# Kernel tuning notes

Measured on AMD Instinct MI355X. Metric: run time of the kernel, lower is better.

The kernel has to match this reference:

```python
import jax, jax.numpy as jnp
import numpy as np
import math

B, T, C = 4, 2048, 768
N_HEADS = 12

def setup_inputs() -> dict:
    key = jax.random.key(0)
    k1, k2, k3 = jax.random.split(key, 3)
    s_in = 1.0 / math.sqrt(C)
    x = jax.random.normal(k1, (B, T, C), dtype=jnp.float32)
    w_attn = jax.random.normal(k2, (C, 3 * C), dtype=jnp.float32) * s_in
    b_attn = jnp.zeros((3 * C,), dtype=jnp.float32)
    w_proj = jax.random.normal(k3, (C, C), dtype=jnp.float32) * s_in
    b_proj = jnp.zeros((C,), dtype=jnp.float32)
    return {"x": x, "w_attn": w_attn, "b_attn": b_attn, "w_proj": w_proj, "b_proj": b_proj}

def reference(x, w_attn, b_attn, w_proj, b_proj):
    Bx, Tx, Cx = x.shape
    hd = Cx // N_HEADS  # head_dim
    qkv = x @ w_attn + b_attn                       # [B,T,3C]
    q, k, v = jnp.split(qkv, 3, axis=-1)
    def heads(t):  # [B,T,C] -> [B,H,T,hd]
        return t.reshape(Bx, Tx, N_HEADS, hd).transpose(0, 2, 1, 3)
    q, k, v = heads(q), heads(k), heads(v)
    scores = jnp.einsum('bhqd,bhkd->bhqk', q, k) * (1.0 / math.sqrt(hd))
    causal = jnp.tril(jnp.ones((Tx, Tx), dtype=bool))
    scores = jnp.where(causal, scores, -jnp.inf)
    attn = jax.nn.softmax(scores, axis=-1)
    out = jnp.einsum('bhqk,bhkd->bhqd', attn, v)    # [B,H,T,hd]
    out = out.transpose(0, 2, 1, 3).reshape(Bx, Tx, Cx)
    return out @ w_proj + b_proj
```

## Files before the change

kernel.cpp:

```cpp
#include <hip/hip_runtime.h>
#include <hip/hip_bf16.h>

typedef __bf16 bf16_8 __attribute__((ext_vector_type(8)));
typedef float f32x4 __attribute__((ext_vector_type(4)));
typedef unsigned short us4 __attribute__((ext_vector_type(4)));

#define AS1(p) ((const __attribute__((address_space(1))) void*)(p))
#define AS3(p) ((__attribute__((address_space(3))) void*)(p))

#define Bb 4
#define Tt 2048
#define Cc 768
#define NH 12
#define HD 64
#define Mrows 8192
#define N1 2304
#define KDIM 768
#define QSCALE 0.1803368801111204f

__device__ __forceinline__ unsigned short bfbits(float x) {
    __bf16 h = (__bf16)x;
    return __builtin_bit_cast(unsigned short, h);
}

__device__ __forceinline__ float exp2fast(float x) {
#if __has_builtin(__builtin_amdgcn_exp2f)
    return __builtin_amdgcn_exp2f(x);
#else
    return __expf(0.6931471805599453f * x);
#endif
}

__global__ __launch_bounds__(256) void cast_f32_bf16(const float* __restrict__ in,
                                                     __bf16* __restrict__ out, int n4) {
    int i = blockIdx.x * blockDim.x + threadIdx.x;
    if (i < n4) {
        float4 v = ((const float4*)in)[i];
        us4 o;
        o.x = bfbits(v.x); o.y = bfbits(v.y); o.z = bfbits(v.z); o.w = bfbits(v.w);
        *(us4*)(out + (size_t)i * 4) = o;
    }
}

__global__ __launch_bounds__(256) void transpose_cast(const float* __restrict__ in,
                                                      __bf16* __restrict__ out, int R, int Cn) {
    __shared__ float tile[32][33];
    int c0 = blockIdx.x * 32, r0 = blockIdx.y * 32;
    int tx = threadIdx.x, ty = threadIdx.y;
#pragma unroll
    for (int i = 0; i < 4; ++i)
        tile[ty + i * 8][tx] = in[(size_t)(r0 + ty + i * 8) * Cn + c0 + tx];
    __syncthreads();
#pragma unroll
    for (int i = 0; i < 4; ++i)
        out[(size_t)(c0 + ty + i * 8) * R + r0 + tx] = (__bf16)tile[tx][ty + i * 8];
}

template <int MODE>
__global__ __launch_bounds__(256) void gemm_bt(const __bf16* __restrict__ A,
                                               const __bf16* __restrict__ Bt,
                                               const float* __restrict__ bias,
                                               float* __restrict__ outf,
                                               __bf16* __restrict__ qb,
                                               __bf16* __restrict__ kb,
                                               __bf16* __restrict__ vTb,
                                               int M, int N, int K) {
    __shared__ __bf16 As[2][128 * 32];
    __shared__ __bf16 Bs[2][128 * 32];
    int tid = threadIdx.x;
    int w = tid >> 6, l = tid & 63, lr = l & 15, lg = l >> 4;
    int wm = w >> 1, wn = w & 1;

    int gx = gridDim.x, gy = gridDim.y;
    int nwg = gx * gy;
    int orig = blockIdx.y * gx + blockIdx.x;
    int q8 = nwg >> 3, r8 = nwg & 7;
    int xcd = orig & 7, rest = orig >> 3;
    int swz = (xcd < r8) ? xcd * (q8 + 1) + rest
                         : r8 * (q8 + 1) + (xcd - r8) * q8 + rest;
    int bx = swz / gy, by = swz % gy;
    int m0 = bx * 128, n0 = by * 128;

    f32x4 acc[4][4] = {};

#define GSTAGE(buf, kk) do {                                                                 \
    _Pragma("unroll")                                                                        \
    for (int i_ = 0; i_ < 2; ++i_) {                                                         \
        int c_ = i_ * 256 + tid;                                                             \
        int row_ = c_ >> 2;                                                                  \
        int jc_ = ((c_ & 3) ^ (row_ & 3)) << 3;                                              \
        __builtin_amdgcn_global_load_lds(AS1(A + (size_t)(m0 + row_) * K + (kk) + jc_),      \
                                         AS3(&As[buf][c_ * 8]), 16, 0, 0);                   \
        __builtin_amdgcn_global_load_lds(AS1(Bt + (size_t)(n0 + row_) * K + (kk) + jc_),     \
                                         AS3(&Bs[buf][c_ * 8]), 16, 0, 0);                   \
    }                                                                                        \
} while (0)

    GSTAGE(0, 0);
    asm volatile("s_waitcnt vmcnt(0)" ::: "memory");
    __builtin_amdgcn_sched_barrier(0);
    __builtin_amdgcn_s_barrier();
    __builtin_amdgcn_sched_barrier(0);

    int nkt = K >> 5;
    for (int kt = 0; kt < nkt; ++kt) {
        int cur = kt & 1;
        if (kt + 1 < nkt) {
            GSTAGE(cur ^ 1, (kt + 1) * 32);
            asm volatile("s_waitcnt vmcnt(4)" ::: "memory");
        } else {
            asm volatile("s_waitcnt vmcnt(0)" ::: "memory");
        }
        __builtin_amdgcn_sched_barrier(0);
        __builtin_amdgcn_s_barrier();
        __builtin_amdgcn_sched_barrier(0);

        const __bf16* Ac = &As[cur][0];
        const __bf16* Bc = &Bs[cur][0];
        bf16_8 af[4], bfr[4];
#pragma unroll
        for (int mi = 0; mi < 4; ++mi)
            af[mi] = *(const bf16_8*)&Ac[(wm * 64 + mi * 16 + lr) * 32 +
                                         ((lg ^ (lr & 3)) << 3)];
#pragma unroll
        for (int ni = 0; ni < 4; ++ni)
            bfr[ni] = *(const bf16_8*)&Bc[(wn * 64 + ni * 16 + lr) * 32 +
                                          ((lg ^ (lr & 3)) << 3)];
#pragma unroll
        for (int mi = 0; mi < 4; ++mi)
#pragma unroll
            for (int ni = 0; ni < 4; ++ni)
                acc[mi][ni] = __builtin_amdgcn_mfma_f32_16x16x32_bf16(af[mi], bfr[ni],
                                                                      acc[mi][ni], 0, 0, 0);
        asm volatile("s_waitcnt lgkmcnt(0)" ::: "memory");
        __builtin_amdgcn_sched_barrier(0);
        __builtin_amdgcn_s_barrier();
        __builtin_amdgcn_sched_barrier(0);
    }

#pragma unroll
    for (int ni = 0; ni < 4; ++ni) {
        int gn = n0 + wn * 64 + ni * 16 + lr;
        float bv = bias[gn];
#pragma unroll
        for (int mi = 0; mi < 4; ++mi) {
            int gm0 = m0 + wm * 64 + mi * 16 + lg * 4;
            f32x4 v = acc[mi][ni];
            if (MODE == 1) {
#pragma unroll
                for (int r = 0; r < 4; ++r)
                    outf[(size_t)(gm0 + r) * N + gn] = v[r] + bv;
            } else {
                int seg = gn / Cc;
                int rem = gn - seg * Cc;
                int h = rem >> 6, d = rem & 63;
                int b = gm0 >> 11, t = gm0 & 2047;
                size_t bh = (size_t)b * NH + h;
                if (seg < 2) {
                    float sc = (seg == 0) ? QSCALE : 1.0f;
                    __bf16* dst = (seg ? kb : qb) + (bh * Tt + t) * HD + d;
#pragma unroll
                    for (int r = 0; r < 4; ++r)
                        dst[(size_t)r * HD] = (__bf16)((v[r] + bv) * sc);
                } else {
                    us4 pk;
#pragma unroll
                    for (int r = 0; r < 4; ++r) pk[r] = bfbits(v[r] + bv);
                    *(us4*)(vTb + (bh * HD + d) * Tt + t) = pk;
                }
            }
        }
    }
}

__global__ __launch_bounds__(256, 2) void attn_fwd(const __bf16* __restrict__ q,
                                                   const __bf16* __restrict__ k,
                                                   const __bf16* __restrict__ vT,
                                                   __bf16* __restrict__ aout) {
    __shared__ __bf16 Ks[2][64 * 64];
    __shared__ __bf16 Vs[2][64 * 64];
    __shared__ __bf16 Ps[4][16 * 64];
    const float NEGINF = -__builtin_inff();

    int blk = blockIdx.x;
    int bh = blk % 48;
    int j = blk / 48;
    int qtA = j, qtB = 31 - j;
    int tid = threadIdx.x;
    int w = tid >> 6, l = tid & 63, lr = l & 15, lg = l >> 4;

    const __bf16* qp = q + (size_t)bh * Tt * HD;
    const __bf16* kp = k + (size_t)bh * Tt * HD;
    const __bf16* vp = vT + (size_t)bh * HD * Tt;

    bf16_8 qfA0, qfA1, qfB0, qfB1;
    {
        int q0A = qtA * 64 + w * 16, q0B = qtB * 64 + w * 16;
        qfA0 = *(const bf16_8*)(qp + (size_t)(q0A + lr) * HD + lg * 8);
        qfA1 = *(const bf16_8*)(qp + (size_t)(q0A + lr) * HD + 32 + lg * 8);
        qfB0 = *(const bf16_8*)(qp + (size_t)(q0B + lr) * HD + lg * 8);
        qfB1 = *(const bf16_8*)(qp + (size_t)(q0B + lr) * HD + 32 + lg * 8);
    }

    f32x4 accOA[4] = {}, accOB[4] = {};
    float sA[4] = {}, sB[4] = {};

    const int swz = lr & 7;
    const int co0 = (lg ^ swz) * 8;
    const int co1 = ((4 + lg) ^ swz) * 8;
    const int qloc = w * 16 + lg * 4;
    __bf16* Pw = &Ps[w][0];

#define STAGE(buf, kvbase) do {                                                              \
    int c0_ = tid, c1_ = 256 + tid;                                                          \
    int row0_ = c0_ >> 3, j0_ = (c0_ & 7) ^ (row0_ & 7);                                     \
    int row1_ = c1_ >> 3, j1_ = (c1_ & 7) ^ (row1_ & 7);                                     \
    __builtin_amdgcn_global_load_lds(AS1(kp + (size_t)((kvbase) + row0_) * HD + j0_ * 8),    \
                                     AS3(&Ks[buf][c0_ * 8]), 16, 0, 0);                      \
    __builtin_amdgcn_global_load_lds(AS1(vp + (size_t)row0_ * Tt + (kvbase) + j0_ * 8),      \
                                     AS3(&Vs[buf][c0_ * 8]), 16, 0, 0);                      \
    __builtin_amdgcn_global_load_lds(AS1(kp + (size_t)((kvbase) + row1_) * HD + j1_ * 8),    \
                                     AS3(&Ks[buf][c1_ * 8]), 16, 0, 0);                      \
    __builtin_amdgcn_global_load_lds(AS1(vp + (size_t)row1_ * Tt + (kvbase) + j1_ * 8),      \
                                     AS3(&Vs[buf][c1_ * 8]), 16, 0, 0);                      \
} while (0)

#define TILE_COMPUTE(qf0, qf1, accO, s, diag) do {                                           \
    f32x4 accS_[4] = {};                                                                     \
    __builtin_amdgcn_s_setprio(1);                                                           \
    _Pragma("unroll")                                                                        \
    for (int nt = 0; nt < 4; ++nt) {                                                         \
        int rb = (nt * 16 + lr) * 64;                                                        \
        bf16_8 kf0_ = *(const bf16_8*)(Kc_ + rb + co0);                                      \
        bf16_8 kf1_ = *(const bf16_8*)(Kc_ + rb + co1);                                      \
        accS_[nt] = __builtin_amdgcn_mfma_f32_16x16x32_bf16(qf0, kf0_, accS_[nt], 0, 0, 0);  \
        accS_[nt] = __builtin_amdgcn_mfma_f32_16x16x32_bf16(qf1, kf1_, accS_[nt], 0, 0, 0);  \
    }                                                                                        \
    __builtin_amdgcn_s_setprio(0);                                                           \
    if (diag) {                                                                              \
        _Pragma("unroll")                                                                    \
        for (int nt = 0; nt < 4; ++nt) {                                                     \
            int kloc_ = nt * 16 + lr;                                                        \
            _Pragma("unroll")                                                                \
            for (int r = 0; r < 4; ++r)                                                      \
                if (kloc_ > qloc + r) accS_[nt][r] = NEGINF;                                 \
        }                                                                                    \
    }                                                                                        \
    _Pragma("unroll")                                                                        \
    for (int r = 0; r < 4; ++r) {                                                            \
        int prow_ = lg * 4 + r;                                                              \
        _Pragma("unroll")                                                                    \
        for (int nt = 0; nt < 4; ++nt) {                                                     \
            float pv_ = exp2fast(accS_[nt][r]);                                              \
            s[r] += pv_;                                                                     \
            int col_ = nt * 16 + lr;                                                         \
            Pw[prow_ * 64 + (((col_ >> 3) ^ (prow_ & 7)) << 3) + (col_ & 7)] = (__bf16)pv_;  \
        }                                                                                    \
    }                                                                                        \
    bf16_8 pf0_ = *(const bf16_8*)&Pw[lr * 64 + ((lg ^ swz) << 3)];                          \
    bf16_8 pf1_ = *(const bf16_8*)&Pw[lr * 64 + (((4 + lg) ^ swz) << 3)];                    \
    __builtin_amdgcn_s_setprio(1);                                                           \
    _Pragma("unroll")                                                                        \
    for (int dt = 0; dt < 4; ++dt) {                                                         \
        int rb = (dt * 16 + lr) * 64;                                                        \
        bf16_8 vf0_ = *(const bf16_8*)(Vc_ + rb + co0);                                      \
        bf16_8 vf1_ = *(const bf16_8*)(Vc_ + rb + co1);                                      \
        accO[dt] = __builtin_amdgcn_mfma_f32_16x16x32_bf16(pf0_, vf0_, accO[dt], 0, 0, 0);   \
        accO[dt] = __builtin_amdgcn_mfma_f32_16x16x32_bf16(pf1_, vf1_, accO[dt], 0, 0, 0);   \
    }                                                                                        \
    __builtin_amdgcn_s_setprio(0);                                                           \
} while (0)

    STAGE(0, 0);
    asm volatile("s_waitcnt vmcnt(0)" ::: "memory");
    __builtin_amdgcn_sched_barrier(0);
    __builtin_amdgcn_s_barrier();
    __builtin_amdgcn_sched_barrier(0);

    for (int kv = 0; kv <= qtB; ++kv) {
        int cur = kv & 1;
        if (kv < qtB) {
            STAGE(cur ^ 1, (kv + 1) * 64);
            asm volatile("s_waitcnt vmcnt(4)" ::: "memory");
        } else {
            asm volatile("s_waitcnt vmcnt(0)" ::: "memory");
        }
        __builtin_amdgcn_sched_barrier(0);
        __builtin_amdgcn_s_barrier();
        __builtin_amdgcn_sched_barrier(0);

        const __bf16* Kc_ = &Ks[cur][0];
        const __bf16* Vc_ = &Vs[cur][0];
        TILE_COMPUTE(qfB0, qfB1, accOB, sB, kv == qtB);
        if (kv <= qtA)
            TILE_COMPUTE(qfA0, qfA1, accOA, sA, kv == qtA);

        asm volatile("s_waitcnt lgkmcnt(0)" ::: "memory");
        __builtin_amdgcn_sched_barrier(0);
        __builtin_amdgcn_s_barrier();
        __builtin_amdgcn_sched_barrier(0);
    }

    int b = bh / NH, h = bh - b * NH;
#define EPILOGUE(accO, s, qt) do {                                                           \
    _Pragma("unroll")                                                                        \
    for (int r = 0; r < 4; ++r) {                                                            \
        float ss_ = s[r];                                                                    \
        _Pragma("unroll")                                                                    \
        for (int off = 1; off < 16; off <<= 1)                                               \
            ss_ += __shfl_xor(ss_, off);                                                     \
        float inv_ = 1.0f / ss_;                                                             \
        size_t row_ = (size_t)(b * Tt + (qt) * 64 + w * 16 + lg * 4 + r) * Cc + h * HD;      \
        _Pragma("unroll")                                                                    \
        for (int dt = 0; dt < 4; ++dt)                                                       \
            aout[row_ + dt * 16 + lr] = (__bf16)(accO[dt][r] * inv_);                        \
    }                                                                                        \
} while (0)

    EPILOGUE(accOA, sA, qtA);
    EPILOGUE(accOB, sB, qtB);
}

extern "C" void kernel_launch(void* const* d_in, const int* in_sizes, int n_in,
                              void* d_out, int out_size, void* d_ws, size_t ws_size,
                              hipStream_t stream) {
    const float* x      = (const float*)d_in[0];
    const float* w_attn = (const float*)d_in[1];
    const float* b_attn = (const float*)d_in[2];
    const float* w_proj = (const float*)d_in[3];
    const float* b_proj = (const float*)d_in[4];
    float* out = (float*)d_out;

    char* ws = (char*)d_ws;
    constexpr size_t SZ_XB   = (size_t)Mrows * KDIM * 2;
    constexpr size_t SZ_WAT  = (size_t)N1 * KDIM * 2;
    constexpr size_t SZ_WPT  = (size_t)Cc * Cc * 2;
    constexpr size_t SZ_HEAD = (size_t)Bb * NH * Tt * HD * 2;
    __bf16* xb  = (__bf16*)ws;
    __bf16* wat = (__bf16*)(ws + SZ_XB);
    __bf16* wpt = (__bf16*)(ws + SZ_XB + SZ_WAT);
    __bf16* qb  = (__bf16*)(ws + SZ_XB + SZ_WAT + SZ_WPT);
    __bf16* kb  = (__bf16*)(ws + SZ_XB + SZ_WAT + SZ_WPT + SZ_HEAD);
    __bf16* vTb = (__bf16*)(ws + SZ_XB + SZ_WAT + SZ_WPT + 2 * SZ_HEAD);
    __bf16* ao  = (__bf16*)(ws + SZ_XB + SZ_WAT + SZ_WPT + 3 * SZ_HEAD);

    cast_f32_bf16<<<(Mrows * KDIM / 4 + 255) / 256, 256, 0, stream>>>(x, xb, Mrows * KDIM / 4);
    transpose_cast<<<dim3(N1 / 32, KDIM / 32), dim3(32, 8), 0, stream>>>(w_attn, wat, KDIM, N1);
    transpose_cast<<<dim3(Cc / 32, Cc / 32), dim3(32, 8), 0, stream>>>(w_proj, wpt, Cc, Cc);

    gemm_bt<0><<<dim3(Mrows / 128, N1 / 128), 256, 0, stream>>>(
        xb, wat, b_attn, nullptr, qb, kb, vTb, Mrows, N1, KDIM);

    attn_fwd<<<48 * 16, 256, 0, stream>>>(qb, kb, vTb, ao);

    gemm_bt<1><<<dim3(Mrows / 128, Cc / 128), 256, 0, stream>>>(
        ao, wpt, b_proj, out, nullptr, nullptr, nullptr, Mrows, Cc, KDIM);
}
```

Baseline: 133.4 us.

## Enlarge attention query tiles to 128 rows and stage QKV epilogue through LDS

The attention kernel now gives each wave 32 query rows instead of 16, so every block covers two 128-row query tiles and the grid is halved. Each K/V tile loaded into LDS is therefore reused across twice as many queries. The causal mask now uses global indices and covers the two diagonal KV tiles. Separately, the QKV GEMM epilogue for the Q and K segments writes through LDS so it can emit 16-byte coalesced stores, replacing scattered 2-byte stores. The cost is higher register pressure, fewer blocks for load balancing, and an extra LDS pass in the GEMM epilogue.

```diff
diff --git a/kernel.cpp b/kernel.cpp
--- a/kernel.cpp
+++ b/kernel.cpp
@@ -65,8 +65,7 @@
                                                __bf16* __restrict__ kb,
                                                __bf16* __restrict__ vTb,
                                                int M, int N, int K) {
-    __shared__ __bf16 As[2][128 * 32];
-    __shared__ __bf16 Bs[2][128 * 32];
+    __shared__ __bf16 SMEM[4][128 * 32];
     int tid = threadIdx.x;
     int w = tid >> 6, l = tid & 63, lr = l & 15, lg = l >> 4;
     int wm = w >> 1, wn = w & 1;
@@ -90,9 +89,9 @@
         int row_ = c_ >> 2;                                                                  \
         int jc_ = ((c_ & 3) ^ (row_ & 3)) << 3;                                              \
         __builtin_amdgcn_global_load_lds(AS1(A + (size_t)(m0 + row_) * K + (kk) + jc_),      \
-                                         AS3(&As[buf][c_ * 8]), 16, 0, 0);                   \
+                                         AS3(&SMEM[buf][c_ * 8]), 16, 0, 0);                 \
         __builtin_amdgcn_global_load_lds(AS1(Bt + (size_t)(n0 + row_) * K + (kk) + jc_),     \
-                                         AS3(&Bs[buf][c_ * 8]), 16, 0, 0);                   \
+                                         AS3(&SMEM[2 + (buf)][c_ * 8]), 16, 0, 0);           \
     }                                                                                        \
 } while (0)
 
@@ -115,8 +114,8 @@
         __builtin_amdgcn_s_barrier();
         __builtin_amdgcn_sched_barrier(0);
 
-        const __bf16* Ac = &As[cur][0];
-        const __bf16* Bc = &Bs[cur][0];
+        const __bf16* Ac = &SMEM[cur][0];
+        const __bf16* Bc = &SMEM[2 + cur][0];
         bf16_8 af[4], bfr[4];
 #pragma unroll
         for (int mi = 0; mi < 4; ++mi)
@@ -138,31 +137,55 @@
         __builtin_amdgcn_sched_barrier(0);
     }
 
-#pragma unroll
-    for (int ni = 0; ni < 4; ++ni) {
-        int gn = n0 + wn * 64 + ni * 16 + lr;
-        float bv = bias[gn];
-#pragma unroll
-        for (int mi = 0; mi < 4; ++mi) {
-            int gm0 = m0 + wm * 64 + mi * 16 + lg * 4;
-            f32x4 v = acc[mi][ni];
-            if (MODE == 1) {
+    int seg = (MODE == 0) ? (n0 / Cc) : 0;
+    if (MODE == 0 && seg < 2) {
+        __bf16* Cs = &SMEM[0][0];
+        float sc = (seg == 0) ? QSCALE : 1.0f;
+#pragma unroll
+        for (int ni = 0; ni < 4; ++ni) {
+            int lnn = wn * 64 + ni * 16 + lr;
+            float bv = bias[n0 + lnn];
+#pragma unroll
+            for (int mi = 0; mi < 4; ++mi) {
+                int lm0 = wm * 64 + mi * 16 + lg * 4;
+                f32x4 v = acc[mi][ni];
 #pragma unroll
                 for (int r = 0; r < 4; ++r)
-                    outf[(size_t)(gm0 + r) * N + gn] = v[r] + bv;
-            } else {
-                int seg = gn / Cc;
-                int rem = gn - seg * Cc;
-                int h = rem >> 6, d = rem & 63;
-                int b = gm0 >> 11, t = gm0 & 2047;
-                size_t bh = (size_t)b * NH + h;
-                if (seg < 2) {
-                    float sc = (seg == 0) ? QSCALE : 1.0f;
-                    __bf16* dst = (seg ? kb : qb) + (bh * Tt + t) * HD + d;
+                    Cs[(lm0 + r) * 128 + lnn] = (__bf16)((v[r] + bv) * sc);
+            }
+        }
+        __builtin_amdgcn_s_barrier();
+        __bf16* base = seg ? kb : qb;
+        int nrem = n0 - seg * Cc;
+#pragma unroll
+        for (int i = 0; i < 8; ++i) {
+            int c = i * 256 + tid;
+            int lm = c >> 4, ln8 = (c & 15) << 3;
+            int t = m0 + lm;
+            int b = t >> 11, tt = t & 2047;
+            int col = nrem + ln8;
+            int h = col >> 6, d = col & 63;
+            *(bf16_8*)(base + ((size_t)(b * NH + h) * Tt + tt) * HD + d) =
+                *(const bf16_8*)&Cs[lm * 128 + ln8];
+        }
+    } else {
+#pragma unroll
+        for (int ni = 0; ni < 4; ++ni) {
+            int gn = n0 + wn * 64 + ni * 16 + lr;
+            float bv = bias[gn];
+#pragma unroll
+            for (int mi = 0; mi < 4; ++mi) {
+                int gm0 = m0 + wm * 64 + mi * 16 + lg * 4;
+                f32x4 v = acc[mi][ni];
+                if (MODE == 1) {
 #pragma unroll
                     for (int r = 0; r < 4; ++r)
-                        dst[(size_t)r * HD] = (__bf16)((v[r] + bv) * sc);
+                        outf[(size_t)(gm0 + r) * N + gn] = v[r] + bv;
                 } else {
+                    int rem = gn - 2 * Cc;
+                    int h = rem >> 6, d = rem & 63;
+                    int b = gm0 >> 11, t = gm0 & 2047;
+                    size_t bh = (size_t)b * NH + h;
                     us4 pk;
 #pragma unroll
                     for (int r = 0; r < 4; ++r) pk[r] = bfbits(v[r] + bv);
@@ -179,36 +202,36 @@
                                                    __bf16* __restrict__ aout) {
     __shared__ __bf16 Ks[2][64 * 64];
     __shared__ __bf16 Vs[2][64 * 64];
-    __shared__ __bf16 Ps[4][16 * 64];
+    __shared__ __bf16 Ps[4][32 * 64];
     const float NEGINF = -__builtin_inff();
 
     int blk = blockIdx.x;
     int bh = blk % 48;
     int j = blk / 48;
-    int qtA = j, qtB = 31 - j;
+    int jA = j, jB = 15 - j;
     int tid = threadIdx.x;
     int w = tid >> 6, l = tid & 63, lr = l & 15, lg = l >> 4;
+    int wb = w * 32;
 
     const __bf16* qp = q + (size_t)bh * Tt * HD;
     const __bf16* kp = k + (size_t)bh * Tt * HD;
     const __bf16* vp = vT + (size_t)bh * HD * Tt;
 
-    bf16_8 qfA0, qfA1, qfB0, qfB1;
-    {
-        int q0A = qtA * 64 + w * 16, q0B = qtB * 64 + w * 16;
-        qfA0 = *(const bf16_8*)(qp + (size_t)(q0A + lr) * HD + lg * 8);
-        qfA1 = *(const bf16_8*)(qp + (size_t)(q0A + lr) * HD + 32 + lg * 8);
-        qfB0 = *(const bf16_8*)(qp + (size_t)(q0B + lr) * HD + lg * 8);
-        qfB1 = *(const bf16_8*)(qp + (size_t)(q0B + lr) * HD + 32 + lg * 8);
-    }
-
-    f32x4 accOA[4] = {}, accOB[4] = {};
-    float sA[4] = {}, sB[4] = {};
+    bf16_8 qfA[2][2], qfB[2][2];
+#pragma unroll
+    for (int mf = 0; mf < 2; ++mf)
+#pragma unroll
+        for (int ks = 0; ks < 2; ++ks) {
+            qfA[mf][ks] = *(const bf16_8*)(qp + (size_t)(jA * 128 + wb + mf * 16 + lr) * HD + ks * 32 + lg * 8);
+            qfB[mf][ks] = *(const bf16_8*)(qp + (size_t)(jB * 128 + wb + mf * 16 + lr) * HD + ks * 32 + lg * 8);
+        }
+
+    f32x4 accOA[2][4] = {}, accOB[2][4] = {};
+    float sA[2][4] = {}, sB[2][4] = {};
 
     const int swz = lr & 7;
     const int co0 = (lg ^ swz) * 8;
     const int co1 = ((4 + lg) ^ swz) * 8;
-    const int qloc = w * 16 + lg * 4;
     __bf16* Pw = &Ps[w][0];
 
 #define STAGE(buf, kvbase) do {                                                              \
@@ -225,48 +248,65 @@
                                      AS3(&Vs[buf][c1_ * 8]), 16, 0, 0);                      \
 } while (0)
 
-#define TILE_COMPUTE(qf0, qf1, accO, s, diag) do {                                           \
-    f32x4 accS_[4] = {};                                                                     \
+#define TILE9(qf, accO, s, qbase, kvb, domask) do {                                          \
+    f32x4 accS_[2][4] = {};                                                                  \
     __builtin_amdgcn_s_setprio(1);                                                           \
     _Pragma("unroll")                                                                        \
     for (int nt = 0; nt < 4; ++nt) {                                                         \
         int rb = (nt * 16 + lr) * 64;                                                        \
         bf16_8 kf0_ = *(const bf16_8*)(Kc_ + rb + co0);                                      \
         bf16_8 kf1_ = *(const bf16_8*)(Kc_ + rb + co1);                                      \
-        accS_[nt] = __builtin_amdgcn_mfma_f32_16x16x32_bf16(qf0, kf0_, accS_[nt], 0, 0, 0);  \
-        accS_[nt] = __builtin_amdgcn_mfma_f32_16x16x32_bf16(qf1, kf1_, accS_[nt], 0, 0, 0);  \
+        _Pragma("unroll")                                                                    \
+        for (int mf = 0; mf < 2; ++mf) {                                                     \
+            accS_[mf][nt] = __builtin_amdgcn_mfma_f32_16x16x32_bf16(qf[mf][0], kf0_, accS_[mf][nt], 0, 0, 0); \
+            accS_[mf][nt] = __builtin_amdgcn_mfma_f32_16x16x32_bf16(qf[mf][1], kf1_, accS_[mf][nt], 0, 0, 0); \
+        }                                                                                    \
     }                                                                                        \
     __builtin_amdgcn_s_setprio(0);                                                           \
-    if (diag) {                                                                              \
+    if (domask) {                                                                            \
         _Pragma("unroll")                                                                    \
         for (int nt = 0; nt < 4; ++nt) {                                                     \
-            int kloc_ = nt * 16 + lr;                                                        \
+            int kg_ = (kvb) + nt * 16 + lr;                                                  \
             _Pragma("unroll")                                                                \
-            for (int r = 0; r < 4; ++r)                                                      \
-                if (kloc_ > qloc + r) accS_[nt][r] = NEGINF;                                 \
+            for (int mf = 0; mf < 2; ++mf) {                                                 \
+                int qg_ = (qbase) + mf * 16 + lg * 4;                                        \
+                _Pragma("unroll")                                                            \
+                for (int r = 0; r < 4; ++r)                                                  \
+                    if (kg_ > qg_ + r) accS_[mf][nt][r] = NEGINF;                            \
+            }                                                                                \
         }                                                                                    \
     }                                                                                        \
     _Pragma("unroll")                                                                        \
-    for (int r = 0; r < 4; ++r) {                                                            \
-        int prow_ = lg * 4 + r;                                                              \
+    for (int mf = 0; mf < 2; ++mf) {                                                         \
         _Pragma("unroll")                                                                    \
-        for (int nt = 0; nt < 4; ++nt) {                                                     \
-            float pv_ = exp2fast(accS_[nt][r]);                                              \
-            s[r] += pv_;                                                                     \
-            int col_ = nt * 16 + lr;                                                         \
-            Pw[prow_ * 64 + (((col_ >> 3) ^ (prow_ & 7)) << 3) + (col_ & 7)] = (__bf16)pv_;  \
+        for (int r = 0; r < 4; ++r) {                                                        \
+            int prow_ = mf * 16 + lg * 4 + r;                                                \
+            _Pragma("unroll")                                                                \
+            for (int nt = 0; nt < 4; ++nt) {                                                 \
+                float pv_ = exp2fast(accS_[mf][nt][r]);                                      \
+                s[mf][r] += pv_;                                                             \
+                int col_ = nt * 16 + lr;                                                     \
+                Pw[prow_ * 64 + (((col_ >> 3) ^ (prow_ & 7)) << 3) + (col_ & 7)] = (__bf16)pv_; \
+            }                                                                                \
         }                                                                                    \
     }                                                                                        \
-    bf16_8 pf0_ = *(const bf16_8*)&Pw[lr * 64 + ((lg ^ swz) << 3)];                          \
-    bf16_8 pf1_ = *(const bf16_8*)&Pw[lr * 64 + (((4 + lg) ^ swz) << 3)];                    \
+    bf16_8 pf_[2][2];                                                                        \
+    _Pragma("unroll")                                                                        \
+    for (int mf = 0; mf < 2; ++mf) {                                                         \
+        pf_[mf][0] = *(const bf16_8*)&Pw[(mf * 16 + lr) * 64 + ((lg ^ swz) << 3)];           \
+        pf_[mf][1] = *(const bf16_8*)&Pw[(mf * 16 + lr) * 64 + (((4 + lg) ^ swz) << 3)];     \
+    }                                                                                        \
     __builtin_amdgcn_s_setprio(1);                                                           \
     _Pragma("unroll")                                                                        \
     for (int dt = 0; dt < 4; ++dt) {                                                         \
         int rb = (dt * 16 + lr) * 64;                                                        \
         bf16_8 vf0_ = *(const bf16_8*)(Vc_ + rb + co0);                                      \
         bf16_8 vf1_ = *(const bf16_8*)(Vc_ + rb + co1);                                      \
-        accO[dt] = __builtin_amdgcn_mfma_f32_16x16x32_bf16(pf0_, vf0_, accO[dt], 0, 0, 0);   \
-        accO[dt] = __builtin_amdgcn_mfma_f32_16x16x32_bf16(pf1_, vf1_, accO[dt], 0, 0, 0);   \
+        _Pragma("unroll")                                                                    \
+        for (int mf = 0; mf < 2; ++mf) {                                                     \
+            accO[mf][dt] = __builtin_amdgcn_mfma_f32_16x16x32_bf16(pf_[mf][0], vf0_, accO[mf][dt], 0, 0, 0); \
+            accO[mf][dt] = __builtin_amdgcn_mfma_f32_16x16x32_bf16(pf_[mf][1], vf1_, accO[mf][dt], 0, 0, 0); \
+        }                                                                                    \
     }                                                                                        \
     __builtin_amdgcn_s_setprio(0);                                                           \
 } while (0)
@@ -277,9 +317,10 @@
     __builtin_amdgcn_s_barrier();
     __builtin_amdgcn_sched_barrier(0);
 
-    for (int kv = 0; kv <= qtB; ++kv) {
+    int nkv = 32 - 2 * j;
+    for (int kv = 0; kv < nkv; ++kv) {
         int cur = kv & 1;
-        if (kv < qtB) {
+        if (kv + 1 < nkv) {
             STAGE(cur ^ 1, (kv + 1) * 64);
             asm volatile("s_waitcnt vmcnt(4)" ::: "memory");
         } else {
@@ -291,9 +332,9 @@
 
         const __bf16* Kc_ = &Ks[cur][0];
         const __bf16* Vc_ = &Vs[cur][0];
-        TILE_COMPUTE(qfB0, qfB1, accOB, sB, kv == qtB);
-        if (kv <= qtA)
-            TILE_COMPUTE(qfA0, qfA1, accOA, sA, kv == qtA);
+        TILE9(qfB, accOB, sB, jB * 128 + wb, kv * 64, kv >= 2 * jB);
+        if (kv <= 2 * jA + 1)
+            TILE9(qfA, accOA, sA, jA * 128 + wb, kv * 64, kv >= 2 * jA);
 
         asm volatile("s_waitcnt lgkmcnt(0)" ::: "memory");
         __builtin_amdgcn_sched_barrier(0);
@@ -302,23 +343,26 @@
     }
 
     int b = bh / NH, h = bh - b * NH;
-#define EPILOGUE(accO, s, qt) do {                                                           \
-    _Pragma("unroll")                                                                        \
-    for (int r = 0; r < 4; ++r) {                                                            \
-        float ss_ = s[r];                                                                    \
+#define EPILOGUE(accO, s, jt) do {                                                           \
+    _Pragma("unroll")                                                                        \
+    for (int mf = 0; mf < 2; ++mf) {                                                         \
         _Pragma("unroll")                                                                    \
-        for (int off = 1; off < 16; off <<= 1)                                               \
-            ss_ += __shfl_xor(ss_, off);                                                     \
-        float inv_ = 1.0f / ss_;                                                             \
-        size_t row_ = (size_t)(b * Tt + (qt) * 64 + w * 16 + lg * 4 + r) * Cc + h * HD;      \
-        _Pragma("unroll")                                                                    \
-        for (int dt = 0; dt < 4; ++dt)                                                       \
-            aout[row_ + dt * 16 + lr] = (__bf16)(accO[dt][r] * inv_);                        \
+        for (int r = 0; r < 4; ++r) {                                                        \
+            float ss_ = s[mf][r];                                                            \
+            _Pragma("unroll")                                                                \
+            for (int off = 1; off < 16; off <<= 1)                                           \
+                ss_ += __shfl_xor(ss_, off);                                                 \
+            float inv_ = 1.0f / ss_;                                                         \
+            size_t row_ = (size_t)(b * Tt + (jt) * 128 + wb + mf * 16 + lg * 4 + r) * Cc + h * HD; \
+            _Pragma("unroll")                                                                \
+            for (int dt = 0; dt < 4; ++dt)                                                   \
+                aout[row_ + dt * 16 + lr] = (__bf16)(accO[mf][dt][r] * inv_);                \
+        }                                                                                    \
     }                                                                                        \
 } while (0)
 
-    EPILOGUE(accOA, sA, qtA);
-    EPILOGUE(accOB, sB, qtB);
+    EPILOGUE(accOA, sA, jA);
+    EPILOGUE(accOB, sB, jB);
 }
 
 extern "C" void kernel_launch(void* const* d_in, const int* in_sizes, int n_in,
@@ -351,7 +395,7 @@
     gemm_bt<0><<<dim3(Mrows / 128, N1 / 128), 256, 0, stream>>>(
         xb, wat, b_attn, nullptr, qb, kb, vTb, Mrows, N1, KDIM);
 
-    attn_fwd<<<48 * 16, 256, 0, stream>>>(qb, kb, vTb, ao);
+    attn_fwd<<<48 * 8, 256, 0, stream>>>(qb, kb, vTb, ao);
 
     gemm_bt<1><<<dim3(Mrows / 128, Cc / 128), 256, 0, stream>>>(
         ao, wpt, b_proj, out, nullptr, nullptr, nullptr, Mrows, Cc, KDIM);
```

After: 137.9 us. 3.4% more time.

## Interleave both query tiles' MFMAs in attention and stage QK epilogue through LDS

Applied to the files above, without the earlier changes.

In the attention loop, the two query tiles (A and B) sharing a K/V block are now processed in one fused macro. Their score and PV MFMAs are interleaved, and a larger P scratch buffer holds both tiles' probabilities. This is meant to give more independent MFMA work per K/V fetch and hide dependency latency, at the cost of more registers and LDS. Separately, the QKV GEMM epilogue for the Q and K segments writes the scaled tile into shared memory first, then stores 16-byte vectors to global, replacing scattered 2-byte stores.

```diff
diff --git a/kernel.cpp b/kernel.cpp
--- a/kernel.cpp
+++ b/kernel.cpp
@@ -65,8 +65,7 @@
                                                __bf16* __restrict__ kb,
                                                __bf16* __restrict__ vTb,
                                                int M, int N, int K) {
-    __shared__ __bf16 As[2][128 * 32];
-    __shared__ __bf16 Bs[2][128 * 32];
+    __shared__ __bf16 SMEM[4][128 * 32];
     int tid = threadIdx.x;
     int w = tid >> 6, l = tid & 63, lr = l & 15, lg = l >> 4;
     int wm = w >> 1, wn = w & 1;
@@ -90,9 +89,9 @@
         int row_ = c_ >> 2;                                                                  \
         int jc_ = ((c_ & 3) ^ (row_ & 3)) << 3;                                              \
         __builtin_amdgcn_global_load_lds(AS1(A + (size_t)(m0 + row_) * K + (kk) + jc_),      \
-                                         AS3(&As[buf][c_ * 8]), 16, 0, 0);                   \
+                                         AS3(&SMEM[buf][c_ * 8]), 16, 0, 0);                 \
         __builtin_amdgcn_global_load_lds(AS1(Bt + (size_t)(n0 + row_) * K + (kk) + jc_),     \
-                                         AS3(&Bs[buf][c_ * 8]), 16, 0, 0);                   \
+                                         AS3(&SMEM[2 + (buf)][c_ * 8]), 16, 0, 0);           \
     }                                                                                        \
 } while (0)
 
@@ -115,8 +114,8 @@
         __builtin_amdgcn_s_barrier();
         __builtin_amdgcn_sched_barrier(0);
 
-        const __bf16* Ac = &As[cur][0];
-        const __bf16* Bc = &Bs[cur][0];
+        const __bf16* Ac = &SMEM[cur][0];
+        const __bf16* Bc = &SMEM[2 + cur][0];
         bf16_8 af[4], bfr[4];
 #pragma unroll
         for (int mi = 0; mi < 4; ++mi)
@@ -138,31 +137,55 @@
         __builtin_amdgcn_sched_barrier(0);
     }
 
-#pragma unroll
-    for (int ni = 0; ni < 4; ++ni) {
-        int gn = n0 + wn * 64 + ni * 16 + lr;
-        float bv = bias[gn];
-#pragma unroll
-        for (int mi = 0; mi < 4; ++mi) {
-            int gm0 = m0 + wm * 64 + mi * 16 + lg * 4;
-            f32x4 v = acc[mi][ni];
-            if (MODE == 1) {
+    int seg = (MODE == 0) ? (n0 / Cc) : 0;
+    if (MODE == 0 && seg < 2) {
+        __bf16* Cs = &SMEM[0][0];
+        float sc = (seg == 0) ? QSCALE : 1.0f;
+#pragma unroll
+        for (int ni = 0; ni < 4; ++ni) {
+            int lnn = wn * 64 + ni * 16 + lr;
+            float bv = bias[n0 + lnn];
+#pragma unroll
+            for (int mi = 0; mi < 4; ++mi) {
+                int lm0 = wm * 64 + mi * 16 + lg * 4;
+                f32x4 v = acc[mi][ni];
 #pragma unroll
                 for (int r = 0; r < 4; ++r)
-                    outf[(size_t)(gm0 + r) * N + gn] = v[r] + bv;
-            } else {
-                int seg = gn / Cc;
-                int rem = gn - seg * Cc;
-                int h = rem >> 6, d = rem & 63;
-                int b = gm0 >> 11, t = gm0 & 2047;
-                size_t bh = (size_t)b * NH + h;
-                if (seg < 2) {
-                    float sc = (seg == 0) ? QSCALE : 1.0f;
-                    __bf16* dst = (seg ? kb : qb) + (bh * Tt + t) * HD + d;
+                    Cs[(lm0 + r) * 128 + lnn] = (__bf16)((v[r] + bv) * sc);
+            }
+        }
+        __builtin_amdgcn_s_barrier();
+        __bf16* base = seg ? kb : qb;
+        int nrem = n0 - seg * Cc;
+#pragma unroll
+        for (int i = 0; i < 8; ++i) {
+            int c = i * 256 + tid;
+            int lm = c >> 4, ln8 = (c & 15) << 3;
+            int t = m0 + lm;
+            int b = t >> 11, tt = t & 2047;
+            int col = nrem + ln8;
+            int h = col >> 6, d = col & 63;
+            *(bf16_8*)(base + ((size_t)(b * NH + h) * Tt + tt) * HD + d) =
+                *(const bf16_8*)&Cs[lm * 128 + ln8];
+        }
+    } else {
+#pragma unroll
+        for (int ni = 0; ni < 4; ++ni) {
+            int gn = n0 + wn * 64 + ni * 16 + lr;
+            float bv = bias[gn];
+#pragma unroll
+            for (int mi = 0; mi < 4; ++mi) {
+                int gm0 = m0 + wm * 64 + mi * 16 + lg * 4;
+                f32x4 v = acc[mi][ni];
+                if (MODE == 1) {
 #pragma unroll
                     for (int r = 0; r < 4; ++r)
-                        dst[(size_t)r * HD] = (__bf16)((v[r] + bv) * sc);
+                        outf[(size_t)(gm0 + r) * N + gn] = v[r] + bv;
                 } else {
+                    int rem = gn - 2 * Cc;
+                    int h = rem >> 6, d = rem & 63;
+                    int b = gm0 >> 11, t = gm0 & 2047;
+                    size_t bh = (size_t)b * NH + h;
                     us4 pk;
 #pragma unroll
                     for (int r = 0; r < 4; ++r) pk[r] = bfbits(v[r] + bv);
@@ -179,7 +202,7 @@
                                                    __bf16* __restrict__ aout) {
     __shared__ __bf16 Ks[2][64 * 64];
     __shared__ __bf16 Vs[2][64 * 64];
-    __shared__ __bf16 Ps[4][16 * 64];
+    __shared__ __bf16 Ps[4][32 * 64];
     const float NEGINF = -__builtin_inff();
 
     int blk = blockIdx.x;
@@ -225,48 +248,102 @@
                                      AS3(&Vs[buf][c1_ * 8]), 16, 0, 0);                      \
 } while (0)
 
-#define TILE_COMPUTE(qf0, qf1, accO, s, diag) do {                                           \
-    f32x4 accS_[4] = {};                                                                     \
+#define TILE_M(maskA) do {                                                                   \
+    f32x4 aS_[2][4] = {};                                                                    \
     __builtin_amdgcn_s_setprio(1);                                                           \
     _Pragma("unroll")                                                                        \
     for (int nt = 0; nt < 4; ++nt) {                                                         \
         int rb = (nt * 16 + lr) * 64;                                                        \
         bf16_8 kf0_ = *(const bf16_8*)(Kc_ + rb + co0);                                      \
         bf16_8 kf1_ = *(const bf16_8*)(Kc_ + rb + co1);                                      \
-        accS_[nt] = __builtin_amdgcn_mfma_f32_16x16x32_bf16(qf0, kf0_, accS_[nt], 0, 0, 0);  \
-        accS_[nt] = __builtin_amdgcn_mfma_f32_16x16x32_bf16(qf1, kf1_, accS_[nt], 0, 0, 0);  \
+        aS_[0][nt] = __builtin_amdgcn_mfma_f32_16x16x32_bf16(qfA0, kf0_, aS_[0][nt], 0, 0, 0); \
+        aS_[1][nt] = __builtin_amdgcn_mfma_f32_16x16x32_bf16(qfB0, kf0_, aS_[1][nt], 0, 0, 0); \
+        aS_[0][nt] = __builtin_amdgcn_mfma_f32_16x16x32_bf16(qfA1, kf1_, aS_[0][nt], 0, 0, 0); \
+        aS_[1][nt] = __builtin_amdgcn_mfma_f32_16x16x32_bf16(qfB1, kf1_, aS_[1][nt], 0, 0, 0); \
     }                                                                                        \
     __builtin_amdgcn_s_setprio(0);                                                           \
-    if (diag) {                                                                              \
+    if (maskA) {                                                                             \
         _Pragma("unroll")                                                                    \
         for (int nt = 0; nt < 4; ++nt) {                                                     \
             int kloc_ = nt * 16 + lr;                                                        \
             _Pragma("unroll")                                                                \
             for (int r = 0; r < 4; ++r)                                                      \
-                if (kloc_ > qloc + r) accS_[nt][r] = NEGINF;                                 \
+                if (kloc_ > qloc + r) aS_[0][nt][r] = NEGINF;                                \
         }                                                                                    \
     }                                                                                        \
     _Pragma("unroll")                                                                        \
     for (int r = 0; r < 4; ++r) {                                                            \
-        int prow_ = lg * 4 + r;                                                              \
+        int prA_ = lg * 4 + r, prB_ = 16 + lg * 4 + r;                                       \
         _Pragma("unroll")                                                                    \
         for (int nt = 0; nt < 4; ++nt) {                                                     \
-            float pv_ = exp2fast(accS_[nt][r]);                                              \
-            s[r] += pv_;                                                                     \
             int col_ = nt * 16 + lr;                                                         \
-            Pw[prow_ * 64 + (((col_ >> 3) ^ (prow_ & 7)) << 3) + (col_ & 7)] = (__bf16)pv_;  \
+            float pvA_ = exp2fast(aS_[0][nt][r]);                                            \
+            float pvB_ = exp2fast(aS_[1][nt][r]);                                            \
+            sA[r] += pvA_; sB[r] += pvB_;                                                    \
+            Pw[prA_ * 64 + (((col_ >> 3) ^ (prA_ & 7)) << 3) + (col_ & 7)] = (__bf16)pvA_;   \
+            Pw[prB_ * 64 + (((col_ >> 3) ^ (prB_ & 7)) << 3) + (col_ & 7)] = (__bf16)pvB_;   \
         }                                                                                    \
     }                                                                                        \
-    bf16_8 pf0_ = *(const bf16_8*)&Pw[lr * 64 + ((lg ^ swz) << 3)];                          \
-    bf16_8 pf1_ = *(const bf16_8*)&Pw[lr * 64 + (((4 + lg) ^ swz) << 3)];                    \
+    bf16_8 pfA0_ = *(const bf16_8*)&Pw[lr * 64 + ((lg ^ swz) << 3)];                         \
+    bf16_8 pfA1_ = *(const bf16_8*)&Pw[lr * 64 + (((4 + lg) ^ swz) << 3)];                   \
+    bf16_8 pfB0_ = *(const bf16_8*)&Pw[(16 + lr) * 64 + ((lg ^ swz) << 3)];                  \
+    bf16_8 pfB1_ = *(const bf16_8*)&Pw[(16 + lr) * 64 + (((4 + lg) ^ swz) << 3)];            \
     __builtin_amdgcn_s_setprio(1);                                                           \
     _Pragma("unroll")                                                                        \
     for (int dt = 0; dt < 4; ++dt) {                                                         \
         int rb = (dt * 16 + lr) * 64;                                                        \
         bf16_8 vf0_ = *(const bf16_8*)(Vc_ + rb + co0);                                      \
         bf16_8 vf1_ = *(const bf16_8*)(Vc_ + rb + co1);                                      \
-        accO[dt] = __builtin_amdgcn_mfma_f32_16x16x32_bf16(pf0_, vf0_, accO[dt], 0, 0, 0);   \
-        accO[dt] = __builtin_amdgcn_mfma_f32_16x16x32_bf16(pf1_, vf1_, accO[dt], 0, 0, 0);   \
+        accOA[dt] = __builtin_amdgcn_mfma_f32_16x16x32_bf16(pfA0_, vf0_, accOA[dt], 0, 0, 0);\
+        accOB[dt] = __builtin_amdgcn_mfma_f32_16x16x32_bf16(pfB0_, vf0_, accOB[dt], 0, 0, 0);\
+        accOA[dt] = __builtin_amdgcn_mfma_f32_16x16x32_bf16(pfA1_, vf1_, accOA[dt], 0, 0, 0);\
+        accOB[dt] = __builtin_amdgcn_mfma_f32_16x16x32_bf16(pfB1_, vf1_, accOB[dt], 0, 0, 0);\
+    }                                                                                        \
+    __builtin_amdgcn_s_setprio(0);                                                           \
+} while (0)
+
+#define TILE_B(maskB) do {                                                                   \
+    f32x4 aS_[4] = {};                                                                       \
+    __builtin_amdgcn_s_setprio(1);                                                           \
+    _Pragma("unroll")                                                                        \
+    for (int nt = 0; nt < 4; ++nt) {                                                         \
+        int rb = (nt * 16 + lr) * 64;                                                        \
+        bf16_8 kf0_ = *(const bf16_8*)(Kc_ + rb + co0);                                      \
+        bf16_8 kf1_ = *(const bf16_8*)(Kc_ + rb + co1);                                      \
+        aS_[nt] = __builtin_amdgcn_mfma_f32_16x16x32_bf16(qfB0, kf0_, aS_[nt], 0, 0, 0);     \
+        aS_[nt] = __builtin_amdgcn_mfma_f32_16x16x32_bf16(qfB1, kf1_, aS_[nt], 0, 0, 0);     \
+    }                                                                                        \
+    __builtin_amdgcn_s_setprio(0);                                                           \
+    if (maskB) {                                                                             \
+        _Pragma("unroll")                                                                    \
+        for (int nt = 0; nt < 4; ++nt) {                                                     \
+            int kloc_ = nt * 16 + lr;                                                        \
+            _Pragma("unroll")                                                                \
+            for (int r = 0; r < 4; ++r)                                                      \
+                if (kloc_ > qloc + r) aS_[nt][r] = NEGINF;                                   \
+        }                                                                                    \
+    }                                                                                        \
+    _Pragma("unroll")                                                                        \
+    for (int r = 0; r < 4; ++r) {                                                            \
+        int prB_ = 16 + lg * 4 + r;                                                          \
+        _Pragma("unroll")                                                                    \
+        for (int nt = 0; nt < 4; ++nt) {                                                     \
+            int col_ = nt * 16 + lr;                                                         \
+            float pv_ = exp2fast(aS_[nt][r]);                                                \
+            sB[r] += pv_;                                                                    \
+            Pw[prB_ * 64 + (((col_ >> 3) ^ (prB_ & 7)) << 3) + (col_ & 7)] = (__bf16)pv_;    \
+        }                                                                                    \
+    }                                                                                        \
+    bf16_8 pf0_ = *(const bf16_8*)&Pw[(16 + lr) * 64 + ((lg ^ swz) << 3)];                   \
+    bf16_8 pf1_ = *(const bf16_8*)&Pw[(16 + lr) * 64 + (((4 + lg) ^ swz) << 3)];             \
+    __builtin_amdgcn_s_setprio(1);                                                           \
+    _Pragma("unroll")                                                                        \
+    for (int dt = 0; dt < 4; ++dt) {                                                         \
+        int rb = (dt * 16 + lr) * 64;                                                        \
+        bf16_8 vf0_ = *(const bf16_8*)(Vc_ + rb + co0);                                      \
+        bf16_8 vf1_ = *(const bf16_8*)(Vc_ + rb + co1);                                      \
+        accOB[dt] = __builtin_amdgcn_mfma_f32_16x16x32_bf16(pf0_, vf0_, accOB[dt], 0, 0, 0); \
+        accOB[dt] = __builtin_amdgcn_mfma_f32_16x16x32_bf16(pf1_, vf1_, accOB[dt], 0, 0, 0); \
     }                                                                                        \
     __builtin_amdgcn_s_setprio(0);                                                           \
 } while (0)
@@ -291,9 +368,10 @@
 
         const __bf16* Kc_ = &Ks[cur][0];
         const __bf16* Vc_ = &Vs[cur][0];
-        TILE_COMPUTE(qfB0, qfB1, accOB, sB, kv == qtB);
         if (kv <= qtA)
-            TILE_COMPUTE(qfA0, qfA1, accOA, sA, kv == qtA);
+            TILE_M(kv == qtA);
+        else
+            TILE_B(kv == qtB);
 
         asm volatile("s_waitcnt lgkmcnt(0)" ::: "memory");
         __builtin_amdgcn_sched_barrier(0);
```

Result: slower. 150.6 us (+12.9%).
